# Performance work log

Measured on AMD Instinct MI355X. Metric: run time of the kernel, lower is better.

Reference implementation:

```python
import jax, jax.numpy as jnp
import numpy as np

V_MIN, V_MAX, ATOMS, GAMMA = -40.0, 80.0, 51, 0.9
BATCH = 524288


def setup_inputs() -> dict:
    key = jax.random.key(0)
    k1, k2, k3 = jax.random.split(key, 3)
    p = jax.random.uniform(k1, (BATCH, ATOMS), dtype=jnp.float32)
    prob_next = p / jnp.sum(p, axis=-1, keepdims=True)  # valid categorical dist
    r = jax.random.normal(k2, (BATCH, 1), dtype=jnp.float32) * 10.0
    done = (jax.random.uniform(k3, (BATCH, 1)) < 0.1).astype(jnp.float32)
    return {"prob_next": prob_next, "r": r, "done": done}


def reference(prob_next, r, done):
    # C51 categorical projection (DistributionalDQN.singleBatch target computation)
    B, A = prob_next.shape
    delta = (V_MAX - V_MIN) / float(A - 1)
    support = jnp.linspace(V_MIN, V_MAX, A, dtype=prob_next.dtype)  # [A]
    atom_next = jnpp_clip = jnp.clip(r + GAMMA * (1.0 - done) * support[None, :], V_MIN, V_MAX)  # [B,A]
    b = (atom_next - V_MIN) / delta
    l = jnp.floor(b)
    u = jnp.ceil(b)
    d_m_l = (u + (l == u).astype(b.dtype) - b) * prob_next
    d_m_u = (b - l) * prob_next
    # vectorized per-row index_add_: flatten rows with offsets and do one scatter-add
    offs = (jnp.arange(B, dtype=jnp.int32) * A)[:, None]  # [B,1]
    li = offs + l.astype(jnp.int32)
    ui = offs + u.astype(jnp.int32)
    flat = jnp.zeros(B * A, dtype=prob_next.dtype)
    flat = flat.at[li.ravel()].add(d_m_l.ravel())
    flat = flat.at[ui.ravel()].add(d_m_u.ravel())
    return flat.reshape(B, A)
```

## Files before the change

kernel.cpp:

```cpp
#include <hip/hip_runtime.h>
#include <stdint.h>


#define ATOMS 51
#define RPB   64
#define THREADS 64
#define TILE_FLOATS (RPB * ATOMS)
#define TILE_VECS   (TILE_FLOATS / 4)
#define STAGE_ITERS ((TILE_VECS + THREADS - 1) / THREADS)
#define GRID_MAX 1536

typedef const __attribute__((address_space(1))) void gvoid_t;
typedef __attribute__((address_space(3))) void lvoid_t;

__device__ __forceinline__ void stage_tile(const float* gbase, float* lbase, int t) {
    #pragma unroll
    for (int i = 0; i < STAGE_ITERS; ++i) {
        const int v = i * THREADS + t;
        if (v < TILE_VECS) {
            __builtin_amdgcn_global_load_lds((gvoid_t*)(gbase + (size_t)v * 4),
                                             (lvoid_t*)(lbase + i * THREADS * 4),
                                             16, 0, 0);
        }
    }
}

__device__ __forceinline__ void compute_row(float* sb, int t, float rr, float dn) {
    const float c = 0.9f * (1.0f - dn);
    const float base = fmaf(-16.66666667f, c, (rr + 40.0f) * (1.0f / 2.4f));
    const int ib = t * ATOMS;

    float p[ATOMS];
    #pragma unroll
    for (int j = 0; j < ATOMS; ++j) p[j] = sb[ib + j];
    #pragma unroll
    for (int j = 0; j < ATOMS; ++j) sb[ib + j] = 0.0f;

    int   cur  = (int)floorf(fminf(fmaxf(base, 0.0f), 50.0f));
    float vcur = 0.0f, vnext = 0.0f;
    #pragma unroll
    for (int j = 0; j < ATOMS; ++j) {
        float b = fmaf(c, (float)j, base);
        b = fminf(fmaxf(b, 0.0f), 50.0f);
        const float lf = floorf(b);
        const float f  = b - lf;
        const int  li  = (int)lf;
        while (li > cur) {
            sb[ib + cur] = vcur;
            vcur = vnext; vnext = 0.0f; ++cur;
        }
        vcur  = fmaf(1.0f - f, p[j], vcur);
        vnext = fmaf(f,        p[j], vnext);
    }
    sb[ib + cur] = vcur;
    if (cur < ATOMS - 1) sb[ib + cur + 1] = vnext;
}

__global__ __launch_bounds__(THREADS) void c51_project(
    const float* __restrict__ prob,
    const float* __restrict__ rin,
    const float* __restrict__ done,
    float* __restrict__ out,
    int nrows)
{
    __shared__ __align__(16) float s_buf[2 * TILE_FLOATS];
    const int t = threadIdx.x;
    const int G = gridDim.x;
    const int ntiles = nrows / RPB;
    const int tail_rows = nrows - ntiles * RPB;

    int tk = blockIdx.x;
    if (tk < ntiles) {
        stage_tile(prob + (size_t)tk * TILE_FLOATS, s_buf, t);
        float rv = rin[(size_t)tk * RPB + t];
        float dv = done[(size_t)tk * RPB + t];
        int buf = 0;

        for (; tk < ntiles; tk += G) {
            const int nxt = tk + G;
            float rnx = 0.0f, dnx = 0.0f;
            if (nxt < ntiles) {
                stage_tile(prob + (size_t)nxt * TILE_FLOATS,
                           s_buf + (buf ^ 1) * TILE_FLOATS, t);
                rnx = rin[(size_t)nxt * RPB + t];
                dnx = done[(size_t)nxt * RPB + t];
                asm volatile("s_waitcnt vmcnt(15)" ::: "memory");
            } else {
                asm volatile("s_waitcnt vmcnt(0)" ::: "memory");
            }
            __builtin_amdgcn_sched_barrier(0);

            float* sb = s_buf + buf * TILE_FLOATS;
            compute_row(sb, t, rv, dv);

            float4* dst = reinterpret_cast<float4*>(out + (size_t)tk * TILE_FLOATS);
            const float4* sv = reinterpret_cast<const float4*>(sb);
            #pragma unroll
            for (int i = 0; i < STAGE_ITERS; ++i) {
                const int v = i * THREADS + t;
                if (v < TILE_VECS) dst[v] = sv[v];
            }

            rv = rnx; dv = dnx;
            buf ^= 1;
        }
    }

    if (tail_rows > 0 && blockIdx.x == 0) {
        const long long row0 = (long long)ntiles * RPB;
        const int n_e = tail_rows * ATOMS;
        const float* gsrc = prob + (size_t)row0 * ATOMS;
        for (int e = t; e < n_e; e += THREADS) s_buf[e] = gsrc[e];
        __syncthreads();
        if (t < tail_rows) compute_row(s_buf, t, rin[row0 + t], done[row0 + t]);
        __syncthreads();
        float* dst = out + (size_t)row0 * ATOMS;
        for (int e = t; e < n_e; e += THREADS) dst[e] = s_buf[e];
    }
}

extern "C" void kernel_launch(void* const* d_in, const int* in_sizes, int n_in,
                              void* d_out, int out_size, void* d_ws, size_t ws_size,
                              hipStream_t stream) {
    const float* prob = (const float*)d_in[0];
    const float* r    = (const float*)d_in[1];
    const float* done = (const float*)d_in[2];
    float* outp = (float*)d_out;
    const int B = in_sizes[1];
    const int ntiles = B / RPB;
    int grid = ntiles < GRID_MAX ? ntiles : GRID_MAX;
    if (grid < 1) grid = 1;
    c51_project<<<dim3(grid), dim3(THREADS), 0, stream>>>(prob, r, done, outp, B);
}
```

Measured before the change: 47.39 us.

## Replace LDS-direct double buffering with register-staged prefetch and single LDS tile

Drops the global_load_lds double-buffered pipeline. The next tile is now prefetched into registers (float4 array) and copied into a single LDS tile each iteration. Halving LDS use and doubling the grid cap is meant to raise occupancy and memory-level parallelism. Row zeroing is now done with float4 stores across the tile, and the inner while becomes an if, since the slope of at most 0.9 advances at most one bin per step. This costs extra VGPRs for staging and relies on single-wave lockstep execution, because there is no barrier between staging and compute.

```diff
diff --git a/kernel.cpp b/kernel.cpp
--- a/kernel.cpp
+++ b/kernel.cpp
@@ -7,23 +7,8 @@
 #define THREADS 64
 #define TILE_FLOATS (RPB * ATOMS)
 #define TILE_VECS   (TILE_FLOATS / 4)
-#define STAGE_ITERS ((TILE_VECS + THREADS - 1) / THREADS)
-#define GRID_MAX 1536
-
-typedef const __attribute__((address_space(1))) void gvoid_t;
-typedef __attribute__((address_space(3))) void lvoid_t;
-
-__device__ __forceinline__ void stage_tile(const float* gbase, float* lbase, int t) {
-    #pragma unroll
-    for (int i = 0; i < STAGE_ITERS; ++i) {
-        const int v = i * THREADS + t;
-        if (v < TILE_VECS) {
-            __builtin_amdgcn_global_load_lds((gvoid_t*)(gbase + (size_t)v * 4),
-                                             (lvoid_t*)(lbase + i * THREADS * 4),
-                                             16, 0, 0);
-        }
-    }
-}
+#define VEC_ITERS   ((TILE_VECS + THREADS - 1) / THREADS)
+#define GRID_MAX 3072
 
 __device__ __forceinline__ void compute_row(float* sb, int t, float rr, float dn) {
     const float c = 0.9f * (1.0f - dn);
@@ -33,8 +18,16 @@
     float p[ATOMS];
     #pragma unroll
     for (int j = 0; j < ATOMS; ++j) p[j] = sb[ib + j];
-    #pragma unroll
-    for (int j = 0; j < ATOMS; ++j) sb[ib + j] = 0.0f;
+
+    {
+        float4* sv = reinterpret_cast<float4*>(sb);
+        const float4 z = make_float4(0.f, 0.f, 0.f, 0.f);
+        #pragma unroll
+        for (int i = 0; i < VEC_ITERS; ++i) {
+            const int v = i * THREADS + t;
+            if (v < TILE_VECS) sv[v] = z;
+        }
+    }
 
     int   cur  = (int)floorf(fminf(fmaxf(base, 0.0f), 50.0f));
     float vcur = 0.0f, vnext = 0.0f;
@@ -45,7 +38,7 @@
         const float lf = floorf(b);
         const float f  = b - lf;
         const int  li  = (int)lf;
-        while (li > cur) {
+        if (li > cur) {
             sb[ib + cur] = vcur;
             vcur = vnext; vnext = 0.0f; ++cur;
         }
@@ -63,7 +56,7 @@
     float* __restrict__ out,
     int nrows)
 {
-    __shared__ __align__(16) float s_buf[2 * TILE_FLOATS];
+    __shared__ __align__(16) float s_buf[TILE_FLOATS];
     const int t = threadIdx.x;
     const int G = gridDim.x;
     const int ntiles = nrows / RPB;
@@ -71,38 +64,55 @@
 
     int tk = blockIdx.x;
     if (tk < ntiles) {
-        stage_tile(prob + (size_t)tk * TILE_FLOATS, s_buf, t);
+        float4 stg[VEC_ITERS];
+        {
+            const float4* gsrc = reinterpret_cast<const float4*>(prob + (size_t)tk * TILE_FLOATS);
+            #pragma unroll
+            for (int i = 0; i < VEC_ITERS; ++i) {
+                const int v = i * THREADS + t;
+                stg[i] = (v < TILE_VECS) ? gsrc[v] : make_float4(0.f, 0.f, 0.f, 0.f);
+            }
+        }
         float rv = rin[(size_t)tk * RPB + t];
         float dv = done[(size_t)tk * RPB + t];
-        int buf = 0;
 
         for (; tk < ntiles; tk += G) {
+            {
+                float4* sv = reinterpret_cast<float4*>(s_buf);
+                #pragma unroll
+                for (int i = 0; i < VEC_ITERS; ++i) {
+                    const int v = i * THREADS + t;
+                    if (v < TILE_VECS) sv[v] = stg[i];
+                }
+            }
+
             const int nxt = tk + G;
             float rnx = 0.0f, dnx = 0.0f;
             if (nxt < ntiles) {
-                stage_tile(prob + (size_t)nxt * TILE_FLOATS,
-                           s_buf + (buf ^ 1) * TILE_FLOATS, t);
+                const float4* gsrc = reinterpret_cast<const float4*>(prob + (size_t)nxt * TILE_FLOATS);
+                #pragma unroll
+                for (int i = 0; i < VEC_ITERS; ++i) {
+                    const int v = i * THREADS + t;
+                    if (v < TILE_VECS) stg[i] = gsrc[v];
+                }
                 rnx = rin[(size_t)nxt * RPB + t];
                 dnx = done[(size_t)nxt * RPB + t];
-                asm volatile("s_waitcnt vmcnt(15)" ::: "memory");
-            } else {
-                asm volatile("s_waitcnt vmcnt(0)" ::: "memory");
             }
             __builtin_amdgcn_sched_barrier(0);
 
-            float* sb = s_buf + buf * TILE_FLOATS;
-            compute_row(sb, t, rv, dv);
+            compute_row(s_buf, t, rv, dv);
 
-            float4* dst = reinterpret_cast<float4*>(out + (size_t)tk * TILE_FLOATS);
-            const float4* sv = reinterpret_cast<const float4*>(sb);
-            #pragma unroll
-            for (int i = 0; i < STAGE_ITERS; ++i) {
-                const int v = i * THREADS + t;
-                if (v < TILE_VECS) dst[v] = sv[v];
+            {
+                float4* dst = reinterpret_cast<float4*>(out + (size_t)tk * TILE_FLOATS);
+                const float4* sv = reinterpret_cast<const float4*>(s_buf);
+                #pragma unroll
+                for (int i = 0; i < VEC_ITERS; ++i) {
+                    const int v = i * THREADS + t;
+                    if (v < TILE_VECS) dst[v] = sv[v];
+                }
             }
 
             rv = rnx; dv = dnx;
-            buf ^= 1;
         }
     }
 
@@ -110,6 +120,7 @@
         const long long row0 = (long long)ntiles * RPB;
         const int n_e = tail_rows * ATOMS;
         const float* gsrc = prob + (size_t)row0 * ATOMS;
+        __syncthreads();
         for (int e = t; e < n_e; e += THREADS) s_buf[e] = gsrc[e];
         __syncthreads();
         if (t < tail_rows) compute_row(s_buf, t, rin[row0 + t], done[row0 + t]);
```

Result: faster. 41.00 us (-13.5%).
